# Performance work log

Hardware: AMD Instinct MI355X
Metric: run time of the kernel (lower is better)

Reference implementation:

```python
import jax, jax.numpy as jnp
import numpy as np

# Hard-coded in the original module: 200 time points over [0, 100]
T_POINTS = jnp.linspace(0.0, 100.0, 200)


def setup_inputs() -> dict:
    key = jax.random.key(0)
    B = 65536
    # params[:,0]=beta, params[:,1]=gamma, params[:,2]=S0, params[:,3]=I0
    params = jax.random.uniform(key, (B, 4), dtype=jnp.float32)
    return {"params": params}


def reference(params):
    # Batched SIR ODE integration on the fixed time grid.
    # Original uses torchdiffeq odeint per sample in a Python loop; here we
    # vectorize across the batch and integrate with classic RK4 on the grid
    # (the SIR RHS is autonomous: t is unused).
    beta, gamma, S0, I0 = params[:, 0], params[:, 1], params[:, 2], params[:, 3]
    R0 = 1.0 - S0 - I0
    y0 = jnp.stack([S0, I0, R0], axis=1)  # [B, 3]

    def rhs(y):  # y: [B, 3]
        S, I = y[:, 0], y[:, 1]
        bSI = beta * S * I
        gI = gamma * I
        return jnp.stack([-bSI, bSI - gI, gI], axis=1)

    dts = T_POINTS[1:] - T_POINTS[:-1]  # [199]

    def step(y, dt):
        k1 = rhs(y)
        k2 = rhs(y + 0.5 * dt * k1)
        k3 = rhs(y + 0.5 * dt * k2)
        k4 = rhs(y + dt * k3)
        y_new = y + (dt / 6.0) * (k1 + 2.0 * k2 + 2.0 * k3 + k4)
        return y_new, y_new

    _, traj = jax.lax.scan(step, y0, dts)            # [199, B, 3]
    full = jnp.concatenate([y0[None], traj], axis=0)  # [200, B, 3]
    return jnp.transpose(full, (1, 0, 2))             # [B, 200, 3]
```

## Files before the change

### kernel.cpp

```cpp
#include <hip/hip_runtime.h>


#define SYS_PER_BLK 64
#define ROW_F   124
#define ROW_F4  31

__global__ __launch_bounds__(64) void sir_rk4_kernel(
    const float* __restrict__ params, float* __restrict__ out)
{
    const int t  = threadIdx.x;
    const int b0 = blockIdx.x * SYS_PER_BLK;
    const int b  = b0 + t;

    __shared__ float lbuf[SYS_PER_BLK * ROW_F];

    const float4 p = reinterpret_cast<const float4*>(params)[b];
    const float beta = p.x, gamma = p.y;
    float S = p.z, I = p.w;
    float R = 1.0f - S - I;

    const float dt = 100.0f / 199.0f;
    const float h2 = 0.5f * dt;
    const float h6 = dt / 6.0f;

    auto step = [&]() {
        float bSI1 = beta * S * I;
        float gI1  = gamma * I;
        float k1S = -bSI1, k1I = bSI1 - gI1, k1R = gI1;
        float S2 = __builtin_fmaf(h2, k1S, S);
        float I2 = __builtin_fmaf(h2, k1I, I);
        float bSI2 = beta * S2 * I2;
        float gI2  = gamma * I2;
        float k2S = -bSI2, k2I = bSI2 - gI2, k2R = gI2;
        float S3 = __builtin_fmaf(h2, k2S, S);
        float I3 = __builtin_fmaf(h2, k2I, I);
        float bSI3 = beta * S3 * I3;
        float gI3  = gamma * I3;
        float k3S = -bSI3, k3I = bSI3 - gI3, k3R = gI3;
        float S4 = __builtin_fmaf(dt, k3S, S);
        float I4 = __builtin_fmaf(dt, k3I, I);
        float bSI4 = beta * S4 * I4;
        float gI4  = gamma * I4;
        float k4S = -bSI4, k4I = bSI4 - gI4, k4R = gI4;
        S = __builtin_fmaf(h6, k1S + 2.0f * (k2S + k3S) + k4S, S);
        I = __builtin_fmaf(h6, k1I + 2.0f * (k2I + k3I) + k4I, I);
        R = __builtin_fmaf(h6, k1R + 2.0f * (k2R + k3R) + k4R, R);
    };

    float4* lrow  = reinterpret_cast<float4*>(&lbuf[t * ROW_F]);
    const float4* lall = reinterpret_cast<const float4*>(lbuf);
    float4* gout  = reinterpret_cast<float4*>(out) + (size_t)b0 * 150;

    for (int c = 0; c < 5; ++c) {
        #pragma unroll
        for (int g = 0; g < 10; ++g) {
            float4 va, vb, vc;
            if (c == 0 && g == 0) { va.x = S; va.y = I; va.z = R; }
            else                  { step(); va.x = S; va.y = I; va.z = R; }
            step(); va.w = S; vb.x = I; vb.y = R;
            step(); vb.z = S; vb.w = I; vc.x = R;
            step(); vc.y = S; vc.z = I; vc.w = R;
            lrow[g * 3 + 0] = va;
            lrow[g * 3 + 1] = vb;
            lrow[g * 3 + 2] = vc;
        }
        #pragma unroll 6
        for (int it = 0; it < 30; ++it) {
            int f = it * 64 + t;
            int r = f / 30;
            int q = f - r * 30;
            float4 v = lall[r * ROW_F4 + q];
            gout[(size_t)r * 150 + c * 30 + q] = v;
        }
    }
}

extern "C" void kernel_launch(void* const* d_in, const int* in_sizes, int n_in,
                              void* d_out, int out_size, void* d_ws, size_t ws_size,
                              hipStream_t stream) {
    const float* params = (const float*)d_in[0];
    float* out = (float*)d_out;
    const int B = in_sizes[0] / 4;
    const int grid = B / SYS_PER_BLK;
    sir_rk4_kernel<<<grid, SYS_PER_BLK, 0, stream>>>(params, out);
}
```

Baseline: 36.36 us.

## Split RK4 integration into checkpoint pass and parallel segment recompute pass

A first kernel integrates each system and saves its state every 20 steps into workspace as checkpoints. A second kernel launches ten times more blocks, one per segment per 64 systems. Each block restarts from its checkpoint, recomputes its 20 steps and writes that slice of the trajectory through shared memory. The goal is more parallelism than 1024 blocks of 64 threads, where a serial 199-step chain per thread leaves the GPU underfilled. The cost is roughly double the arithmetic, an extra launch, and checkpoint traffic. The old fused kernel remains as a fallback when the workspace is too small.

```diff
diff --git a/kernel.cpp b/kernel.cpp
--- a/kernel.cpp
+++ b/kernel.cpp
@@ -1,75 +1,132 @@
 #include <hip/hip_runtime.h>
 
 
-#define SYS_PER_BLK 64
-#define ROW_F   124
-#define ROW_F4  31
+#define SEG   20
+#define NSEG  10
+#define ROW_F 68
 
-__global__ __launch_bounds__(64) void sir_rk4_kernel(
-    const float* __restrict__ params, float* __restrict__ out)
+__device__ __forceinline__ void rk4_step(float beta, float gamma,
+                                         float& S, float& I, float& R)
 {
-    const int t  = threadIdx.x;
-    const int b0 = blockIdx.x * SYS_PER_BLK;
-    const int b  = b0 + t;
+    const float dt = 100.0f / 199.0f;
+    const float h2 = 0.5f * dt;
+    const float h6 = dt / 6.0f;
+    float bSI1 = beta * S * I;
+    float gI1  = gamma * I;
+    float k1S = -bSI1, k1I = bSI1 - gI1, k1R = gI1;
+    float S2 = __builtin_fmaf(h2, k1S, S);
+    float I2 = __builtin_fmaf(h2, k1I, I);
+    float bSI2 = beta * S2 * I2;
+    float gI2  = gamma * I2;
+    float k2S = -bSI2, k2I = bSI2 - gI2, k2R = gI2;
+    float S3 = __builtin_fmaf(h2, k2S, S);
+    float I3 = __builtin_fmaf(h2, k2I, I);
+    float bSI3 = beta * S3 * I3;
+    float gI3  = gamma * I3;
+    float k3S = -bSI3, k3I = bSI3 - gI3, k3R = gI3;
+    float S4 = __builtin_fmaf(dt, k3S, S);
+    float I4 = __builtin_fmaf(dt, k3I, I);
+    float bSI4 = beta * S4 * I4;
+    float gI4  = gamma * I4;
+    float k4S = -bSI4, k4I = bSI4 - gI4, k4R = gI4;
+    S = __builtin_fmaf(h6, k1S + 2.0f * (k2S + k3S) + k4S, S);
+    I = __builtin_fmaf(h6, k1I + 2.0f * (k2I + k3I) + k4I, I);
+    R = __builtin_fmaf(h6, k1R + 2.0f * (k2R + k3R) + k4R, R);
+}
 
-    __shared__ float lbuf[SYS_PER_BLK * ROW_F];
-
+__global__ __launch_bounds__(256) void sir_pass1(
+    const float* __restrict__ params, float4* __restrict__ cp, int B)
+{
+    const int b = blockIdx.x * 256 + threadIdx.x;
     const float4 p = reinterpret_cast<const float4*>(params)[b];
     const float beta = p.x, gamma = p.y;
     float S = p.z, I = p.w;
     float R = 1.0f - S - I;
+    #pragma unroll 1
+    for (int k = 0; k < NSEG - 1; ++k) {
+        #pragma unroll 4
+        for (int j = 0; j < SEG; ++j) rk4_step(beta, gamma, S, I, R);
+        cp[k * B + b] = make_float4(S, I, R, 0.0f);
+    }
+}
 
-    const float dt = 100.0f / 199.0f;
-    const float h2 = 0.5f * dt;
-    const float h6 = dt / 6.0f;
+__global__ __launch_bounds__(64) void sir_pass2(
+    const float* __restrict__ params, const float4* __restrict__ cp,
+    float* __restrict__ out, int B)
+{
+    const int bid = blockIdx.x;
+    const int s = bid % NSEG;
+    const int i = bid / NSEG;
+    const int t = threadIdx.x;
+    const int b = i * 64 + t;
 
-    auto step = [&]() {
-        float bSI1 = beta * S * I;
-        float gI1  = gamma * I;
-        float k1S = -bSI1, k1I = bSI1 - gI1, k1R = gI1;
-        float S2 = __builtin_fmaf(h2, k1S, S);
-        float I2 = __builtin_fmaf(h2, k1I, I);
-        float bSI2 = beta * S2 * I2;
-        float gI2  = gamma * I2;
-        float k2S = -bSI2, k2I = bSI2 - gI2, k2R = gI2;
-        float S3 = __builtin_fmaf(h2, k2S, S);
-        float I3 = __builtin_fmaf(h2, k2I, I);
-        float bSI3 = beta * S3 * I3;
-        float gI3  = gamma * I3;
-        float k3S = -bSI3, k3I = bSI3 - gI3, k3R = gI3;
-        float S4 = __builtin_fmaf(dt, k3S, S);
-        float I4 = __builtin_fmaf(dt, k3I, I);
-        float bSI4 = beta * S4 * I4;
-        float gI4  = gamma * I4;
-        float k4S = -bSI4, k4I = bSI4 - gI4, k4R = gI4;
-        S = __builtin_fmaf(h6, k1S + 2.0f * (k2S + k3S) + k4S, S);
-        I = __builtin_fmaf(h6, k1I + 2.0f * (k2I + k3I) + k4I, I);
-        R = __builtin_fmaf(h6, k1R + 2.0f * (k2R + k3R) + k4R, R);
-    };
+    __shared__ float lbuf[64 * ROW_F];
 
-    float4* lrow  = reinterpret_cast<float4*>(&lbuf[t * ROW_F]);
-    const float4* lall = reinterpret_cast<const float4*>(lbuf);
-    float4* gout  = reinterpret_cast<float4*>(out) + (size_t)b0 * 150;
+    const float4 p = reinterpret_cast<const float4*>(params)[b];
+    const float beta = p.x, gamma = p.y;
+    float S, I, R;
+    if (s == 0) { S = p.z; I = p.w; R = 1.0f - S - I; }
+    else        { float4 c = cp[(s - 1) * B + b]; S = c.x; I = c.y; R = c.z; }
 
+    float4* lrow = reinterpret_cast<float4*>(&lbuf[t * ROW_F]);
+    {
+        float4 va, vb, vc;
+        va.x = S; va.y = I; va.z = R;
+        rk4_step(beta, gamma, S, I, R); va.w = S; vb.x = I; vb.y = R;
+        rk4_step(beta, gamma, S, I, R); vb.z = S; vb.w = I; vc.x = R;
+        rk4_step(beta, gamma, S, I, R); vc.y = S; vc.z = I; vc.w = R;
+        lrow[0] = va; lrow[1] = vb; lrow[2] = vc;
+        #pragma unroll
+        for (int g = 1; g < 5; ++g) {
+            rk4_step(beta, gamma, S, I, R); va.x = S; va.y = I; va.z = R;
+            rk4_step(beta, gamma, S, I, R); va.w = S; vb.x = I; vb.y = R;
+            rk4_step(beta, gamma, S, I, R); vb.z = S; vb.w = I; vc.x = R;
+            rk4_step(beta, gamma, S, I, R); vc.y = S; vc.z = I; vc.w = R;
+            lrow[g * 3 + 0] = va; lrow[g * 3 + 1] = vb; lrow[g * 3 + 2] = vc;
+        }
+    }
+
+    float4* gout = reinterpret_cast<float4*>(out) + (size_t)i * 64 * 150 + s * 15;
+    #pragma unroll 5
+    for (int it = 0; it < 15; ++it) {
+        int f = it * 64 + t;
+        int r = f / 15;
+        int q = f - r * 15;
+        float4 v = *reinterpret_cast<const float4*>(&lbuf[r * ROW_F + q * 4]);
+        gout[(size_t)r * 150 + q] = v;
+    }
+}
+
+#define FB_ROW_F  124
+__global__ __launch_bounds__(64) void sir_fused(
+    const float* __restrict__ params, float* __restrict__ out)
+{
+    const int t  = threadIdx.x;
+    const int b0 = blockIdx.x * 64;
+    __shared__ float lbuf[64 * FB_ROW_F];
+    const float4 p = reinterpret_cast<const float4*>(params)[b0 + t];
+    const float beta = p.x, gamma = p.y;
+    float S = p.z, I = p.w;
+    float R = 1.0f - S - I;
+    float4* lrow = reinterpret_cast<float4*>(&lbuf[t * FB_ROW_F]);
+    float4* gout = reinterpret_cast<float4*>(out) + (size_t)b0 * 150;
     for (int c = 0; c < 5; ++c) {
         #pragma unroll
         for (int g = 0; g < 10; ++g) {
             float4 va, vb, vc;
             if (c == 0 && g == 0) { va.x = S; va.y = I; va.z = R; }
-            else                  { step(); va.x = S; va.y = I; va.z = R; }
-            step(); va.w = S; vb.x = I; vb.y = R;
-            step(); vb.z = S; vb.w = I; vc.x = R;
-            step(); vc.y = S; vc.z = I; vc.w = R;
-            lrow[g * 3 + 0] = va;
-            lrow[g * 3 + 1] = vb;
-            lrow[g * 3 + 2] = vc;
+            else { rk4_step(beta, gamma, S, I, R); va.x = S; va.y = I; va.z = R; }
+            rk4_step(beta, gamma, S, I, R); va.w = S; vb.x = I; vb.y = R;
+            rk4_step(beta, gamma, S, I, R); vb.z = S; vb.w = I; vc.x = R;
+            rk4_step(beta, gamma, S, I, R); vc.y = S; vc.z = I; vc.w = R;
+            lrow[g * 3 + 0] = va; lrow[g * 3 + 1] = vb; lrow[g * 3 + 2] = vc;
         }
         #pragma unroll 6
         for (int it = 0; it < 30; ++it) {
             int f = it * 64 + t;
             int r = f / 30;
             int q = f - r * 30;
-            float4 v = lall[r * ROW_F4 + q];
+            float4 v = *reinterpret_cast<const float4*>(&lbuf[r * FB_ROW_F + q * 4]);
             gout[(size_t)r * 150 + c * 30 + q] = v;
         }
     }
@@ -81,6 +138,12 @@
     const float* params = (const float*)d_in[0];
     float* out = (float*)d_out;
     const int B = in_sizes[0] / 4;
-    const int grid = B / SYS_PER_BLK;
-    sir_rk4_kernel<<<grid, SYS_PER_BLK, 0, stream>>>(params, out);
+    const size_t cp_bytes = (size_t)(NSEG - 1) * B * 16;
+    if (ws_size >= cp_bytes) {
+        float4* cp = (float4*)d_ws;
+        sir_pass1<<<B / 256, 256, 0, stream>>>(params, cp, B);
+        sir_pass2<<<(B / 64) * NSEG, 64, 0, stream>>>(params, cp, out, B);
+    } else {
+        sir_fused<<<B / 64, 64, 0, stream>>>(params, out);
+    }
 }
```

Measured after the change: 55.90 us. 53.8% more time.
